# Performance work log

Hardware: AMD Instinct MI355X
Metric: run time of the kernel (lower is better)

The kernel has to match this reference:

```python
import jax, jax.numpy as jnp
import numpy as np

B, S, D, C, H = 4, 2048, 1024, 2, 16
LN_EPS = 1e-5


def setup_inputs() -> dict:
    key = jax.random.key(0)
    ks = jax.random.split(key, 6)
    return {
        "token_emb": jax.random.normal(ks[0], (B, S, D), dtype=jnp.float32),
        "chunk_w": jax.random.normal(ks[1], (D, C * D), dtype=jnp.float32) * 0.02,
        "chunk_b": jnp.zeros((D,), dtype=jnp.float32),
        "in_proj_w": jax.random.normal(ks[2], (3 * D, D), dtype=jnp.float32) * 0.02,
        "in_proj_b": jnp.zeros((3 * D,), dtype=jnp.float32),
        "out_proj_w": jax.random.normal(ks[3], (D, D), dtype=jnp.float32) * 0.02,
        "out_proj_b": jnp.zeros((D,), dtype=jnp.float32),
        "ln_g": jnp.ones((D,), dtype=jnp.float32),
        "ln_b": jnp.zeros((D,), dtype=jnp.float32),
        "num_heads": H,
    }


def _layer_norm(x, g, b):
    mu = jnp.mean(x, axis=-1, keepdims=True)
    var = jnp.mean((x - mu) ** 2, axis=-1, keepdims=True)
    return (x - mu) * jax.lax.rsqrt(var + LN_EPS) * g + b


def reference(token_emb, chunk_w, chunk_b, in_proj_w, in_proj_b,
              out_proj_w, out_proj_b, ln_g, ln_b, num_heads):
    Bq, Sq, Dq = token_emb.shape
    c = chunk_w.shape[1] // Dq
    # Sliding windows with zero padding at the end (vectorized unfold).
    padded = jnp.pad(token_emb, ((0, 0), (0, c - 1), (0, 0)))
    # (B, S, c*D): concat the c shifted views along feature dim
    windows = jnp.concatenate([padded[:, k:k + Sq, :] for k in range(c)], axis=-1)
    chunk = jnp.einsum('bsf,df->bsd', windows, chunk_w) + chunk_b  # (B,S,D)

    # Multi-head self-attention (torch nn.MultiheadAttention semantics).
    qkv = jnp.einsum('bsd,ed->bse', chunk, in_proj_w) + in_proj_b
    q, k, v = jnp.split(qkv, 3, axis=-1)
    dh = Dq // num_heads
    q = q.reshape(Bq, Sq, num_heads, dh)
    k = k.reshape(Bq, Sq, num_heads, dh)
    v = v.reshape(Bq, Sq, num_heads, dh)
    scores = jnp.einsum('bqhd,bkhd->bhqk', q, k) / jnp.sqrt(jnp.float32(dh))
    probs = jax.nn.softmax(scores, axis=-1)
    attn = jnp.einsum('bhqk,bkhd->bqhd', probs, v).reshape(Bq, Sq, Dq)
    attn = jnp.einsum('bsd,ed->bse', attn, out_proj_w) + out_proj_b

    return _layer_norm(chunk + attn, ln_g, ln_b)
```

## Files before the change

### kernel.cpp

```cpp
#include <hip/hip_runtime.h>


typedef __bf16 bf16x8 __attribute__((ext_vector_type(8)));
typedef float f32x4 __attribute__((ext_vector_type(4)));
typedef float f32x16 __attribute__((ext_vector_type(16)));

#if __has_builtin(__builtin_amdgcn_exp2f)
#define EXP2(x) __builtin_amdgcn_exp2f(x)
#else
#define EXP2(x) exp2f(x)
#endif

__device__ __forceinline__ unsigned short f2bf(float x) {
  unsigned u = __float_as_uint(x);
  u += 0x7fffu + ((u >> 16) & 1u);
  return (unsigned short)(u >> 16);
}

__device__ __forceinline__ float bf2f(unsigned short x) {
  return __uint_as_float(((unsigned)x) << 16);
}

__device__ __forceinline__ void glds16(const ushort* g, ushort* l) {
  __builtin_amdgcn_global_load_lds(
      (const __attribute__((address_space(1))) unsigned int*)g,
      (__attribute__((address_space(3))) unsigned int*)l, 16, 0, 0);
}

__global__ __launch_bounds__(256) void build_awin(const float* __restrict__ emb,
                                                  ushort* __restrict__ aw) {
  const int i = blockIdx.x * 256 + threadIdx.x;
  const int e = i * 4;
  const int m = e >> 11;
  const int k = e & 2047;
  float4 v;
  if (k < 1024) {
    v = *(const float4*)(emb + (size_t)m * 1024 + k);
  } else {
    const int s = m & 2047;
    if (s == 2047) v = make_float4(0.f, 0.f, 0.f, 0.f);
    else           v = *(const float4*)(emb + (size_t)(m + 1) * 1024 + (k - 1024));
  }
  ushort4 o;
  o.x = f2bf(v.x); o.y = f2bf(v.y); o.z = f2bf(v.z); o.w = f2bf(v.w);
  *(ushort4*)(aw + (size_t)e) = o;
}

__global__ __launch_bounds__(256) void cvt_bf16(const float* __restrict__ in,
                                                ushort* __restrict__ out, int n4) {
  const int i = blockIdx.x * 256 + threadIdx.x;
  if (i >= n4) return;
  float4 v = ((const float4*)in)[i];
  ushort4 o;
  o.x = f2bf(v.x); o.y = f2bf(v.y); o.z = f2bf(v.z); o.w = f2bf(v.w);
  ((ushort4*)out)[i] = o;
}

__global__ __launch_bounds__(256) void gemm_bt(
    const ushort* __restrict__ A, const ushort* __restrict__ W,
    const float* __restrict__ bias, int M, int N, int K, int mode,
    float* __restrict__ outf, ushort* __restrict__ outb,
    const ushort* __restrict__ residb) {
  __shared__ __align__(16) ushort sA[8192];
  __shared__ __align__(16) ushort sB[8192];
  const int t = threadIdx.x, wave = t >> 6, lane = t & 63;
  const int c16 = lane & 15, quad = lane >> 4;
  const int wm = wave >> 1, wn = wave & 1;
  const int m0 = blockIdx.x * 128, n0 = blockIdx.y * 128;
  f32x4 acc[4][4] = {};
  const ushort* gA[4];
  const ushort* gB[4];
  ushort* lA[4];
  ushort* lB[4];
#pragma unroll
  for (int c = 0; c < 4; ++c) {
    const int j = wave * 4 + c;
    const int ks = j >> 1, row = (j & 1) * 64 + lane;
    gA[c] = A + (size_t)(m0 + row) * K + ks * 8;
    gB[c] = W + (size_t)(n0 + row) * K + ks * 8;
    lA[c] = sA + j * 512;
    lB[c] = sB + j * 512;
  }
  for (int k0 = 0; k0 < K; k0 += 64) {
    __syncthreads();
#pragma unroll
    for (int c = 0; c < 4; ++c) {
      glds16(gA[c] + k0, lA[c]);
      glds16(gB[c] + k0, lB[c]);
    }
    __syncthreads();
#pragma unroll
    for (int kc = 0; kc < 2; ++kc) {
      bf16x8 af[4], bfr[4];
#pragma unroll
      for (int i = 0; i < 4; ++i) {
        af[i]  = *(const bf16x8*)(sA + ((kc * 4 + quad) * 128 + wm * 64 + i * 16 + c16) * 8);
        bfr[i] = *(const bf16x8*)(sB + ((kc * 4 + quad) * 128 + wn * 64 + i * 16 + c16) * 8);
      }
#pragma unroll
      for (int mt = 0; mt < 4; ++mt)
#pragma unroll
        for (int nt = 0; nt < 4; ++nt)
          acc[mt][nt] = __builtin_amdgcn_mfma_f32_16x16x32_bf16(af[mt], bfr[nt],
                                                                acc[mt][nt], 0, 0, 0);
    }
  }
  const float QS = 0.18033688011112042f;
  float bv[4];
#pragma unroll
  for (int nt = 0; nt < 4; ++nt) bv[nt] = bias[n0 + wn * 64 + nt * 16 + c16];
#pragma unroll
  for (int mt = 0; mt < 4; ++mt) {
#pragma unroll
    for (int nt = 0; nt < 4; ++nt) {
      const int n = n0 + wn * 64 + nt * 16 + c16;
#pragma unroll
      for (int r = 0; r < 4; ++r) {
        const int m = m0 + wm * 64 + mt * 16 + quad * 4 + r;
        const size_t idx = (size_t)m * N + n;
        float v = acc[mt][nt][r] + bv[nt];
        if (mode == 2)      { outf[idx] = v + bf2f(residb[idx]); }
        else {
          if (mode == 1 && n < 1024) v *= QS;
          outb[idx] = f2bf(v);
        }
      }
    }
  }
}

__global__ __launch_bounds__(256) void vtrans(const ushort* __restrict__ qkv,
                                              ushort* __restrict__ vt) {
  const int sb = blockIdx.x, h = blockIdx.y, b = blockIdx.z;
  __shared__ ushort tile[64][72];
  const int t = threadIdx.x;
  {
    const int row = t >> 3, c8 = (t & 7) * 8;
    const ushort* src = qkv + (size_t)(b * 2048 + sb * 64 + row) * 3072 + 2048 + h * 64 + c8;
    *(uint4*)&tile[row][c8]      = *(const uint4*)src;
    *(uint4*)&tile[row + 32][c8] = *(const uint4*)(src + 32 * 3072);
  }
  __syncthreads();
  const int d = t >> 2, seg = (t & 3) * 16;
  unsigned wbuf[8];
#pragma unroll
  for (int i = 0; i < 8; ++i)
    wbuf[i] = (unsigned)tile[seg + 2 * i][d] | ((unsigned)tile[seg + 2 * i + 1][d] << 16);
  ushort* dst = vt + (size_t)((b * 16 + h) * 64 + d) * 2048 + sb * 64 + seg;
  *(uint4*)(dst)     = *(uint4*)&wbuf[0];
  *(uint4*)(dst + 8) = *(uint4*)&wbuf[4];
}

__global__ __launch_bounds__(256, 4) void attn_kernel(
    const ushort* __restrict__ qkv, const ushort* __restrict__ vtp,
    ushort* __restrict__ attn_out) {
  const int S = 2048;
  const int bh = blockIdx.x, qblk = blockIdx.y;
  const int h = bh & 15, b = bh >> 4;
  const int t = threadIdx.x, wave = t >> 6, lane = t & 63;
  const int c32 = lane & 31, hi = lane >> 5;
  __shared__ __align__(16) ushort sK[8192];
  __shared__ __align__(16) ushort sV[8192];
  const int q0 = qblk * 128;
  const size_t qrow = (size_t)(b * S + q0 + wave * 32 + c32);
  const int swv0 = (c32 ^ (c32 >> 3)) & 15;
  const int dv1 = 32 + c32;
  const int swv1 = (dv1 ^ (dv1 >> 3)) & 15;
  bf16x8 qf[4];
  {
    const ushort* qp = qkv + qrow * 3072 + h * 64 + hi * 8;
#pragma unroll
    for (int dk = 0; dk < 4; ++dk) qf[dk] = *(const bf16x8*)(qp + dk * 16);
  }
  f32x16 o0 = {}, o1 = {};
  float li = 0.f;
  const int j0 = wave * 4;

  for (int kv0 = 0; kv0 < S; kv0 += 128) {
    __syncthreads();
#pragma unroll
    for (int c = 0; c < 4; ++c) {
      const int j = j0 + c;
      const int dslot = j >> 1, key = (j & 1) * 64 + lane;
      glds16(qkv + (size_t)(b * S + kv0 + key) * 3072 + 1024 + h * 64 + dslot * 8,
             sK + j * 512);
      const int d = j * 4 + (lane >> 4);
      const int ksv = (lane & 15) ^ ((d ^ (d >> 3)) & 15);
      glds16(vtp + (size_t)((b * 16 + h) * 64 + d) * S + kv0 + ksv * 8,
             sV + j * 512);
    }
    __syncthreads();
#pragma unroll
    for (int kt = 0; kt < 4; ++kt) {
      f32x16 z = {};
#pragma unroll
      for (int dk = 0; dk < 4; ++dk) {
        bf16x8 kf = *(const bf16x8*)(sK + ((dk * 2 + hi) * 128 + kt * 32 + c32) * 8);
        z = __builtin_amdgcn_mfma_f32_32x32x16_bf16(kf, qf[dk], z, 0, 0, 0);
      }
      uint2 w[4];
#pragma unroll
      for (int g = 0; g < 4; ++g) {
        const float p0 = EXP2(z[g * 4 + 0]);
        const float p1 = EXP2(z[g * 4 + 1]);
        const float p2 = EXP2(z[g * 4 + 2]);
        const float p3 = EXP2(z[g * 4 + 3]);
        li += (p0 + p1) + (p2 + p3);
        w[g].x = __builtin_amdgcn_perm(__float_as_uint(p1), __float_as_uint(p0),
                                       0x07060302u);
        w[g].y = __builtin_amdgcn_perm(__float_as_uint(p3), __float_as_uint(p2),
                                       0x07060302u);
      }
      uint2 pp[4];
#pragma unroll
      for (int g = 0; g < 4; ++g) {
        pp[g].x = __shfl_xor((int)w[g].x, 32);
        pp[g].y = __shfl_xor((int)w[g].y, 32);
      }
#pragma unroll
      for (int e = 0; e < 2; ++e) {
        const uint2 lo4 = hi ? pp[2 * e + 1] : w[2 * e];
        const uint2 hi4 = hi ? w[2 * e + 1] : pp[2 * e];
        const uint4 fr = make_uint4(lo4.x, lo4.y, hi4.x, hi4.y);
        bf16x8 pf;
        __builtin_memcpy(&pf, &fr, 16);
        const int ksl = kt * 4 + e * 2 + hi;
        bf16x8 vf0 = *(const bf16x8*)(sV + (c32 * 16 + (ksl ^ swv0)) * 8);
        o0 = __builtin_amdgcn_mfma_f32_32x32x16_bf16(vf0, pf, o0, 0, 0, 0);
        bf16x8 vf1 = *(const bf16x8*)(sV + (dv1 * 16 + (ksl ^ swv1)) * 8);
        o1 = __builtin_amdgcn_mfma_f32_32x32x16_bf16(vf1, pf, o1, 0, 0, 0);
      }
    }
  }
  li += __shfl_xor(li, 32);
  const float inv = 1.f / li;
  ushort* orow = attn_out + qrow * 1024 + h * 64;
#pragma unroll
  for (int dt = 0; dt < 2; ++dt) {
    const f32x16 ov = dt ? o1 : o0;
#pragma unroll
    for (int g = 0; g < 4; ++g) {
      float v0 = ov[g * 4 + 0] * inv, v1 = ov[g * 4 + 1] * inv;
      float v2 = ov[g * 4 + 2] * inv, v3 = ov[g * 4 + 3] * inv;
      uint2 w2;
      w2.x = (unsigned)f2bf(v0) | ((unsigned)f2bf(v1) << 16);
      w2.y = (unsigned)f2bf(v2) | ((unsigned)f2bf(v3) << 16);
      *(uint2*)(orow + dt * 32 + g * 8 + hi * 4) = w2;
    }
  }
}

__global__ __launch_bounds__(256) void ln_kernel(const float* __restrict__ y,
                                                 const float* __restrict__ g,
                                                 const float* __restrict__ bta,
                                                 float* __restrict__ out) {
  const int m = blockIdx.x;
  const int t = threadIdx.x;
  const float* row = y + (size_t)m * 1024;
  float4 v = ((const float4*)row)[t];
  float s = v.x + v.y + v.z + v.w;
  float s2 = v.x * v.x + v.y * v.y + v.z * v.z + v.w * v.w;
#pragma unroll
  for (int off = 1; off < 64; off <<= 1) {
    s += __shfl_xor(s, off, 64);
    s2 += __shfl_xor(s2, off, 64);
  }
  __shared__ float red[8];
  const int wave = t >> 6, lane = t & 63;
  if (lane == 0) { red[wave] = s; red[4 + wave] = s2; }
  __syncthreads();
  s = red[0] + red[1] + red[2] + red[3];
  s2 = red[4] + red[5] + red[6] + red[7];
  const float mu = s * (1.f / 1024.f);
  const float var = s2 * (1.f / 1024.f) - mu * mu;
  const float rs = rsqrtf(var + 1e-5f);
  float4 gg = ((const float4*)g)[t];
  float4 bb = ((const float4*)bta)[t];
  float4 o;
  o.x = (v.x - mu) * rs * gg.x + bb.x;
  o.y = (v.y - mu) * rs * gg.y + bb.y;
  o.z = (v.z - mu) * rs * gg.z + bb.z;
  o.w = (v.w - mu) * rs * gg.w + bb.w;
  ((float4*)(out + (size_t)m * 1024))[t] = o;
}

extern "C" void kernel_launch(void* const* d_in, const int* in_sizes, int n_in,
                              void* d_out, int out_size, void* d_ws, size_t ws_size,
                              hipStream_t stream) {
  const float* emb        = (const float*)d_in[0];
  const float* chunk_w    = (const float*)d_in[1];
  const float* chunk_b    = (const float*)d_in[2];
  const float* in_proj_w  = (const float*)d_in[3];
  const float* in_proj_b  = (const float*)d_in[4];
  const float* out_proj_w = (const float*)d_in[5];
  const float* out_proj_b = (const float*)d_in[6];
  const float* ln_g       = (const float*)d_in[7];
  const float* ln_b       = (const float*)d_in[8];

  char* w = (char*)d_ws;
  const size_t MBy = (size_t)1 << 20;
  ushort* qkvb   = (ushort*)(w + 0);
  ushort* awin   = (ushort*)(w + 0);
  float*  y      = (float*)(w + 0);
  ushort* chunkb = (ushort*)(w + 48 * MBy);
  ushort* vtb    = (ushort*)(w + 64 * MBy);
  ushort* attnb  = (ushort*)(w + 80 * MBy);
  ushort* cwb    = (ushort*)(w + 96 * MBy);
  ushort* ipwb   = (ushort*)(w + 100 * MBy);
  ushort* opwb   = (ushort*)(w + 106 * MBy);

  build_awin<<<16384, 256, 0, stream>>>(emb, awin);
  cvt_bf16<<<2048, 256, 0, stream>>>(chunk_w, cwb, 2 * 1024 * 1024 / 4);
  cvt_bf16<<<3072, 256, 0, stream>>>(in_proj_w, ipwb, 3 * 1024 * 1024 / 4);
  cvt_bf16<<<1024, 256, 0, stream>>>(out_proj_w, opwb, 1024 * 1024 / 4);

  gemm_bt<<<dim3(8192 / 128, 1024 / 128), 256, 0, stream>>>(
      awin, cwb, chunk_b, 8192, 1024, 2048, 0, nullptr, chunkb, nullptr);

  gemm_bt<<<dim3(8192 / 128, 3072 / 128), 256, 0, stream>>>(
      chunkb, ipwb, in_proj_b, 8192, 3072, 1024, 1, nullptr, qkvb, nullptr);

  vtrans<<<dim3(32, 16, 4), 256, 0, stream>>>(qkvb, vtb);

  attn_kernel<<<dim3(64, 2048 / 128, 1), 256, 0, stream>>>(qkvb, vtb, attnb);

  gemm_bt<<<dim3(8192 / 128, 1024 / 128), 256, 0, stream>>>(
      attnb, opwb, out_proj_b, 8192, 1024, 1024, 2, y, nullptr, chunkb);

  ln_kernel<<<8192, 256, 0, stream>>>(y, ln_g, ln_b, (float*)d_out);
}
```

Baseline: 469.5 us.

## Process two query tiles per wave in attention and drop P shuffles

Each wave now handles 64 query rows as two 32-row tiles, so every K/V tile staged in shared memory and every K fragment read from LDS is reused across twice as many queries. The grid is halved to match. The PV product switches to the 32x32x8 bf16 MFMA, which uses the per-lane P layout directly and removes the cross-half shuffle. In exchange, register pressure doubles, the occupancy hint drops from 4 to 3 blocks, and there are fewer blocks to spread across CUs.

```diff
diff --git a/kernel.cpp b/kernel.cpp
--- a/kernel.cpp
+++ b/kernel.cpp
@@ -4,6 +4,8 @@
 typedef __bf16 bf16x8 __attribute__((ext_vector_type(8)));
 typedef float f32x4 __attribute__((ext_vector_type(4)));
 typedef float f32x16 __attribute__((ext_vector_type(16)));
+typedef short s16x4 __attribute__((ext_vector_type(4)));
+typedef __bf16 b16x4 __attribute__((ext_vector_type(4)));
 
 #if __has_builtin(__builtin_amdgcn_exp2f)
 #define EXP2(x) __builtin_amdgcn_exp2f(x)
@@ -19,6 +21,20 @@
 
 __device__ __forceinline__ float bf2f(unsigned short x) {
   return __uint_as_float(((unsigned)x) << 16);
+}
+
+__device__ __forceinline__ f32x16 mfma328(uint2 a, uint2 b, f32x16 c) {
+#if __has_builtin(__builtin_amdgcn_mfma_f32_32x32x8_bf16)
+  b16x4 av, bv;
+  __builtin_memcpy(&av, &a, 8);
+  __builtin_memcpy(&bv, &b, 8);
+  return __builtin_amdgcn_mfma_f32_32x32x8_bf16(av, bv, c, 0, 0, 0);
+#else
+  s16x4 av, bv;
+  __builtin_memcpy(&av, &a, 8);
+  __builtin_memcpy(&bv, &b, 8);
+  return __builtin_amdgcn_mfma_f32_32x32x8bf16_1k(av, bv, c, 0, 0, 0);
+#endif
 }
 
 __device__ __forceinline__ void glds16(const ushort* g, ushort* l) {
@@ -151,7 +167,7 @@
   *(uint4*)(dst + 8) = *(uint4*)&wbuf[4];
 }
 
-__global__ __launch_bounds__(256, 4) void attn_kernel(
+__global__ __launch_bounds__(256, 3) void attn_kernel(
     const ushort* __restrict__ qkv, const ushort* __restrict__ vtp,
     ushort* __restrict__ attn_out) {
   const int S = 2048;
@@ -161,19 +177,24 @@
   const int c32 = lane & 31, hi = lane >> 5;
   __shared__ __align__(16) ushort sK[8192];
   __shared__ __align__(16) ushort sV[8192];
-  const int q0 = qblk * 128;
-  const size_t qrow = (size_t)(b * S + q0 + wave * 32 + c32);
+  const int q0 = qblk * 256;
+  const size_t qrow_a = (size_t)(b * S + q0 + wave * 64 + c32);
+  const size_t qrow_b = qrow_a + 32;
   const int swv0 = (c32 ^ (c32 >> 3)) & 15;
   const int dv1 = 32 + c32;
   const int swv1 = (dv1 ^ (dv1 >> 3)) & 15;
-  bf16x8 qf[4];
+  bf16x8 qfa[4], qfb[4];
   {
-    const ushort* qp = qkv + qrow * 3072 + h * 64 + hi * 8;
-#pragma unroll
-    for (int dk = 0; dk < 4; ++dk) qf[dk] = *(const bf16x8*)(qp + dk * 16);
-  }
-  f32x16 o0 = {}, o1 = {};
-  float li = 0.f;
+    const ushort* qpa = qkv + qrow_a * 3072 + h * 64 + hi * 8;
+    const ushort* qpb = qkv + qrow_b * 3072 + h * 64 + hi * 8;
+#pragma unroll
+    for (int dk = 0; dk < 4; ++dk) {
+      qfa[dk] = *(const bf16x8*)(qpa + dk * 16);
+      qfb[dk] = *(const bf16x8*)(qpb + dk * 16);
+    }
+  }
+  f32x16 o0a = {}, o1a = {}, o0b = {}, o1b = {};
+  float lia = 0.f, lib = 0.f;
   const int j0 = wave * 4;
 
   for (int kv0 = 0; kv0 < S; kv0 += 128) {
@@ -192,60 +213,67 @@
     __syncthreads();
 #pragma unroll
     for (int kt = 0; kt < 4; ++kt) {
-      f32x16 z = {};
+      bf16x8 kf[4];
+#pragma unroll
+      for (int dk = 0; dk < 4; ++dk)
+        kf[dk] = *(const bf16x8*)(sK + ((dk * 2 + hi) * 128 + kt * 32 + c32) * 8);
+      f32x16 za = {}, zb = {};
 #pragma unroll
       for (int dk = 0; dk < 4; ++dk) {
-        bf16x8 kf = *(const bf16x8*)(sK + ((dk * 2 + hi) * 128 + kt * 32 + c32) * 8);
-        z = __builtin_amdgcn_mfma_f32_32x32x16_bf16(kf, qf[dk], z, 0, 0, 0);
-      }
-      uint2 w[4];
+        za = __builtin_amdgcn_mfma_f32_32x32x16_bf16(kf[dk], qfa[dk], za, 0, 0, 0);
+        zb = __builtin_amdgcn_mfma_f32_32x32x16_bf16(kf[dk], qfb[dk], zb, 0, 0, 0);
+      }
+      uint2 wa[4], wb[4];
 #pragma unroll
       for (int g = 0; g < 4; ++g) {
-        const float p0 = EXP2(z[g * 4 + 0]);
-        const float p1 = EXP2(z[g * 4 + 1]);
-        const float p2 = EXP2(z[g * 4 + 2]);
-        const float p3 = EXP2(z[g * 4 + 3]);
-        li += (p0 + p1) + (p2 + p3);
-        w[g].x = __builtin_amdgcn_perm(__float_as_uint(p1), __float_as_uint(p0),
-                                       0x07060302u);
-        w[g].y = __builtin_amdgcn_perm(__float_as_uint(p3), __float_as_uint(p2),
-                                       0x07060302u);
-      }
-      uint2 pp[4];
+        float pa0 = EXP2(za[g * 4 + 0]), pa1 = EXP2(za[g * 4 + 1]);
+        float pa2 = EXP2(za[g * 4 + 2]), pa3 = EXP2(za[g * 4 + 3]);
+        lia += (pa0 + pa1) + (pa2 + pa3);
+        wa[g].x = __builtin_amdgcn_perm(__float_as_uint(pa1), __float_as_uint(pa0),
+                                        0x07060302u);
+        wa[g].y = __builtin_amdgcn_perm(__float_as_uint(pa3), __float_as_uint(pa2),
+                                        0x07060302u);
+        float pb0 = EXP2(zb[g * 4 + 0]), pb1 = EXP2(zb[g * 4 + 1]);
+        float pb2 = EXP2(zb[g * 4 + 2]), pb3 = EXP2(zb[g * 4 + 3]);
+        lib += (pb0 + pb1) + (pb2 + pb3);
+        wb[g].x = __builtin_amdgcn_perm(__float_as_uint(pb1), __float_as_uint(pb0),
+                                        0x07060302u);
+        wb[g].y = __builtin_amdgcn_perm(__float_as_uint(pb3), __float_as_uint(pb2),
+                                        0x07060302u);
+      }
 #pragma unroll
       for (int g = 0; g < 4; ++g) {
-        pp[g].x = __shfl_xor((int)w[g].x, 32);
-        pp[g].y = __shfl_xor((int)w[g].y, 32);
-      }
-#pragma unroll
-      for (int e = 0; e < 2; ++e) {
-        const uint2 lo4 = hi ? pp[2 * e + 1] : w[2 * e];
-        const uint2 hi4 = hi ? w[2 * e + 1] : pp[2 * e];
-        const uint4 fr = make_uint4(lo4.x, lo4.y, hi4.x, hi4.y);
-        bf16x8 pf;
-        __builtin_memcpy(&pf, &fr, 16);
-        const int ksl = kt * 4 + e * 2 + hi;
-        bf16x8 vf0 = *(const bf16x8*)(sV + (c32 * 16 + (ksl ^ swv0)) * 8);
-        o0 = __builtin_amdgcn_mfma_f32_32x32x16_bf16(vf0, pf, o0, 0, 0, 0);
-        bf16x8 vf1 = *(const bf16x8*)(sV + (dv1 * 16 + (ksl ^ swv1)) * 8);
-        o1 = __builtin_amdgcn_mfma_f32_32x32x16_bf16(vf1, pf, o1, 0, 0, 0);
-      }
-    }
-  }
-  li += __shfl_xor(li, 32);
-  const float inv = 1.f / li;
-  ushort* orow = attn_out + qrow * 1024 + h * 64;
-#pragma unroll
-  for (int dt = 0; dt < 2; ++dt) {
-    const f32x16 ov = dt ? o1 : o0;
-#pragma unroll
-    for (int g = 0; g < 4; ++g) {
-      float v0 = ov[g * 4 + 0] * inv, v1 = ov[g * 4 + 1] * inv;
-      float v2 = ov[g * 4 + 2] * inv, v3 = ov[g * 4 + 3] * inv;
-      uint2 w2;
-      w2.x = (unsigned)f2bf(v0) | ((unsigned)f2bf(v1) << 16);
-      w2.y = (unsigned)f2bf(v2) | ((unsigned)f2bf(v3) << 16);
-      *(uint2*)(orow + dt * 32 + g * 8 + hi * 4) = w2;
+        const int ksl = kt * 4 + g;
+        uint2 va0 = *(const uint2*)(sV + (c32 * 16 + (ksl ^ swv0)) * 8 + hi * 4);
+        uint2 va1 = *(const uint2*)(sV + (dv1 * 16 + (ksl ^ swv1)) * 8 + hi * 4);
+        o0a = mfma328(va0, wa[g], o0a);
+        o1a = mfma328(va1, wa[g], o1a);
+        o0b = mfma328(va0, wb[g], o0b);
+        o1b = mfma328(va1, wb[g], o1b);
+      }
+    }
+  }
+  lia += __shfl_xor(lia, 32);
+  lib += __shfl_xor(lib, 32);
+  const float inva = 1.f / lia, invb = 1.f / lib;
+  ushort* orow_a = attn_out + qrow_a * 1024 + h * 64;
+  ushort* orow_b = attn_out + qrow_b * 1024 + h * 64;
+#pragma unroll
+  for (int half = 0; half < 2; ++half) {
+    ushort* orow = half ? orow_b : orow_a;
+    const float inv = half ? invb : inva;
+#pragma unroll
+    for (int dt = 0; dt < 2; ++dt) {
+      const f32x16 ov = half ? (dt ? o1b : o0b) : (dt ? o1a : o0a);
+#pragma unroll
+      for (int g = 0; g < 4; ++g) {
+        float v0 = ov[g * 4 + 0] * inv, v1 = ov[g * 4 + 1] * inv;
+        float v2 = ov[g * 4 + 2] * inv, v3 = ov[g * 4 + 3] * inv;
+        uint2 w2;
+        w2.x = (unsigned)f2bf(v0) | ((unsigned)f2bf(v1) << 16);
+        w2.y = (unsigned)f2bf(v2) | ((unsigned)f2bf(v3) << 16);
+        *(uint2*)(orow + dt * 32 + g * 8 + hi * 4) = w2;
+      }
     }
   }
 }
@@ -322,7 +350,7 @@
 
   vtrans<<<dim3(32, 16, 4), 256, 0, stream>>>(qkvb, vtb);
 
-  attn_kernel<<<dim3(64, 2048 / 128, 1), 256, 0, stream>>>(qkvb, vtb, attnb);
+  attn_kernel<<<dim3(64, 2048 / 256, 1), 256, 0, stream>>>(qkvb, vtb, attnb);
 
   gemm_bt<<<dim3(8192 / 128, 1024 / 128), 256, 0, stream>>>(
       attnb, opwb, out_proj_b, 8192, 1024, 1024, 2, y, nullptr, chunkb);
```

Result: slower. 743.8 us (+58.4%).
